# Kernel optimization log

Hardware: AMD Instinct MI355X
Metric: run time of the kernel (lower is better)

The kernel has to match this reference:

```python
import jax, jax.numpy as jnp
import numpy as np

NSLICES = 4
HID = 512
IN_DIM = 342   # input_shape - 1 (last column is phase)
OUT_DIM = 311
BATCH = 1024


def _cubic(y0, y1, y2, y3, mu):
    mu2 = mu * mu
    mu3 = mu2 * mu
    return ((-0.5 * y0 + 1.5 * y1 - 1.5 * y2 + 0.5 * y3) * mu3
            + (y0 - 2.5 * y1 + 2.0 * y2 - 0.5 * y3) * mu2
            + (-0.5 * y0 + 0.5 * y2) * mu
            + y1)


def setup_inputs() -> dict:
    key = jax.random.key(0)
    kx, k0, k1, k2 = jax.random.split(key, 4)
    x = jax.random.uniform(kx, (BATCH, IN_DIM + 1), dtype=jnp.float32)
    W0 = jax.random.normal(k0, (NSLICES, HID, IN_DIM), dtype=jnp.float32) * 0.1
    W1 = jax.random.normal(k1, (NSLICES, HID, HID), dtype=jnp.float32) * 0.1
    W2 = jax.random.normal(k2, (NSLICES, OUT_DIM, HID), dtype=jnp.float32) * 0.1
    b0 = jnp.zeros((NSLICES, HID), dtype=jnp.float32)
    b1 = jnp.zeros((NSLICES, HID), dtype=jnp.float32)
    b2 = jnp.zeros((NSLICES, OUT_DIM), dtype=jnp.float32)
    return {"x": x, "W0": W0, "W1": W1, "W2": W2, "b0": b0, "b1": b1, "b2": b2}


def reference(x, W0, W1, W2, b0, b1, b2):
    data, phase = x[:, :-1], x[:, -1]          # [B, 342], [B]
    pscale = NSLICES * phase                    # phase in [0,1) -> pscale in [0,4)
    mu = pscale % 1.0                           # [B]
    i1 = pscale.astype(jnp.int32) % NSLICES
    i0 = (i1 - 1) % NSLICES
    i2 = (i1 + 1) % NSLICES
    i3 = (i1 + 2) % NSLICES

    muW = mu[:, None, None]
    mub = mu[:, None]

    # Per-sample interpolated weights/biases (gather 4 slices + cubic blend)
    W0i = _cubic(W0[i0], W0[i1], W0[i2], W0[i3], muW)   # [B, 512, 342]
    W1i = _cubic(W1[i0], W1[i1], W1[i2], W1[i3], muW)   # [B, 512, 512]
    W2i = _cubic(W2[i0], W2[i1], W2[i2], W2[i3], muW)   # [B, 311, 512]
    b0i = _cubic(b0[i0], b0[i1], b0[i2], b0[i3], mub)   # [B, 512]
    b1i = _cubic(b1[i0], b1[i1], b1[i2], b1[i3], mub)   # [B, 512]
    b2i = _cubic(b2[i0], b2[i1], b2[i2], b2[i3], mub)   # [B, 311]

    # 3-layer MLP with per-sample weights (batched GEMV); dropout in eval mode (identity)
    H1 = jax.nn.elu(jnp.einsum('boi,bi->bo', W0i, data) + b0i)
    H2 = jax.nn.elu(jnp.einsum('boi,bi->bo', W1i, H1) + b1i)
    H3 = jnp.einsum('boi,bi->bo', W2i, H2) + b2i
    return H3
```

## Files before the change

### kernel.cpp

```cpp
#include <hip/hip_runtime.h>
#include <hip/hip_fp16.h>
#include <math.h>

typedef _Float16 f16x8 __attribute__((ext_vector_type(8)));
typedef float f32x4 __attribute__((ext_vector_type(4)));

#define NS 4
#define HID 512
#define IN_DIM 342
#define OUT_DIM 311
#define BATCH 1024
#define INP 352
#define K0V (NS*INP)
#define K12V (NS*HID)
#define XROW (IN_DIM+1)

#define OFF_ACOEF 0
#define OFF_X0H   4096
#define OFF_W0H   (OFF_X0H + 720896)
#define OFF_W1H   (OFF_W0H + 360448)
#define OFF_W2H   (OFF_W1H + 524288)
#define OFF_H1X   (OFF_W2H + 327680)
#define OFF_H2X   OFF_X0H

typedef __attribute__((address_space(3))) void lds_t;
typedef __attribute__((address_space(1))) const void gvm_t;
__device__ __forceinline__ void gload16(const void* g, void* l) {
    __builtin_amdgcn_global_load_lds((gvm_t*)g, (lds_t*)l, 16, 0, 0);
}

__global__ __launch_bounds__(256) void prep_all(
    const float* __restrict__ x,
    const float* __restrict__ W0, const float* __restrict__ W1,
    const float* __restrict__ W2,
    float* __restrict__ acoef,
    __half* __restrict__ X0h, __half* __restrict__ W0h,
    __half* __restrict__ W1h, __half* __restrict__ W2h)
{
    const int bid = blockIdx.x;
    const int t = threadIdx.x;
    if (bid < 512) {
        int o = bid;
        for (int k = t; k < K0V; k += 256) {
            int s = k / INP;
            int i = k - s*INP;
            float v = 0.f;
            if (i < IN_DIM) v = W0[((size_t)s*HID + o)*IN_DIM + i];
            W0h[(size_t)o*K0V + k] = __float2half(v);
        }
    } else if (bid < 1024) {
        int o = bid - 512;
        int k = t * 8;
        int s = k >> 9, i = k & 511;
        const float* src = W1 + ((size_t)s*HID + o)*HID + i;
        float4 v0 = *(const float4*)(src);
        float4 v1 = *(const float4*)(src + 4);
        f16x8 h;
        h[0]=(_Float16)v0.x; h[1]=(_Float16)v0.y; h[2]=(_Float16)v0.z; h[3]=(_Float16)v0.w;
        h[4]=(_Float16)v1.x; h[5]=(_Float16)v1.y; h[6]=(_Float16)v1.z; h[7]=(_Float16)v1.w;
        *(f16x8*)(W1h + (size_t)o*K12V + k) = h;
    } else if (bid < 1344) {
        int o = bid - 1024;
        int k = t * 8;
        int s = k >> 9, i = k & 511;
        f16x8 h = {};
        if (o < OUT_DIM) {
            const float* src = W2 + ((size_t)s*OUT_DIM + o)*HID + i;
            float4 v0 = *(const float4*)(src);
            float4 v1 = *(const float4*)(src + 4);
            h[0]=(_Float16)v0.x; h[1]=(_Float16)v0.y; h[2]=(_Float16)v0.z; h[3]=(_Float16)v0.w;
            h[4]=(_Float16)v1.x; h[5]=(_Float16)v1.y; h[6]=(_Float16)v1.z; h[7]=(_Float16)v1.w;
        }
        *(f16x8*)(W2h + (size_t)o*K12V + k) = h;
    } else {
        int b = bid - 1344;
        float phase = x[(size_t)b*XROW + IN_DIM];
        float ps = (float)NS * phase;
        float mu = ps - floorf(ps);
        int i1 = ((int)ps) & (NS-1);
        float mu2 = mu*mu, mu3 = mu2*mu;
        float c1 =  1.5f*mu3 - 2.5f*mu2 + 1.0f;
        float c2 = -1.5f*mu3 + 2.0f*mu2 + 0.5f*mu;
        float c3 =  0.5f*mu3 - 0.5f*mu2;
        float c0 = -0.5f*mu3 +      mu2 - 0.5f*mu;
        if (t < 4) {
            int rel = (t - i1) & 3;
            acoef[b*4 + t] = (rel==0)?c1:(rel==1)?c2:(rel==2)?c3:c0;
        }
        for (int k = t; k < K0V; k += 256) {
            int s = k / INP;
            int i = k - s*INP;
            int rel = (s - i1) & 3;
            float sel = (rel==0)?c1:(rel==1)?c2:(rel==2)?c3:c0;
            float v = (i < IN_DIM) ? x[(size_t)b*XROW + i] * sel : 0.f;
            X0h[(size_t)b*K0V + k] = __float2half(v);
        }
    }
}

template<int LAYER>
__global__ __launch_bounds__(256) void gemm_mfma(
    const __half* __restrict__ A,
    const __half* __restrict__ Bw,
    const float* __restrict__ acoef,
    const float* __restrict__ bias,
    __half* __restrict__ outH,
    float* __restrict__ outF)
{
    constexpr int K  = (LAYER==0) ? K0V : K12V;
    constexpr int NB = (LAYER==2) ? OUT_DIM : HID;
    constexpr int NITER = K / 64;

    __shared__ __align__(16) char lbuf[4][12288];

    const int t    = threadIdx.x;
    const int lane = t & 63;
    const int wid  = t >> 6;
    const int wm   = wid >> 1;
    const int wn   = wid & 1;
    const int m0   = blockIdx.y * 32;
    const int n0   = blockIdx.x * 64;

    const int rA = t >> 3, cA = t & 7;
    const __half* aSrc = A + (size_t)(m0 + rA)*K + ((cA ^ (rA & 7)) * 8);
    const __half* bSrc0 = Bw + (size_t)(n0 + rA)*K      + ((cA ^ (rA & 7)) * 8);
    const __half* bSrc1 = Bw + (size_t)(n0 + 32 + rA)*K + ((cA ^ (rA & 7)) * 8);
    const int wb = wid * 1024;

    f32x4 acc[2] = {};

    auto stage = [&](int it) {
        char* base = lbuf[it & 3];
        const int ko = it * 64;
        gload16(aSrc  + ko, base        + wb);
        gload16(bSrc0 + ko, base + 4096 + wb);
        gload16(bSrc1 + ko, base + 8192 + wb);
    };

    stage(0);
    stage(1);
    stage(2);

    for (int it = 0; it < NITER; ++it) {
        if (it + 2 < NITER)      asm volatile("s_waitcnt vmcnt(6)" ::: "memory");
        else if (it + 1 < NITER) asm volatile("s_waitcnt vmcnt(3)" ::: "memory");
        else                     asm volatile("s_waitcnt vmcnt(0)" ::: "memory");
        __builtin_amdgcn_s_barrier();
        __builtin_amdgcn_sched_barrier(0);
        if (it + 3 < NITER) stage(it + 3);
        const char* sA = lbuf[it & 3];
        const char* sB = sA + 4096;
        #pragma unroll
        for (int kk = 0; kk < 2; ++kk) {
            const int kb = kk*64 + (lane>>4)*16;
            const int rr = wm*16 + (lane&15);
            f16x8 af = *(const f16x8*)(sA + rr*128 + (kb ^ ((rr&7)<<4)));
            #pragma unroll
            for (int ni = 0; ni < 2; ++ni) {
                const int oo = wn*32 + ni*16 + (lane&15);
                f16x8 bf = *(const f16x8*)(sB + oo*128 + (kb ^ ((oo&7)<<4)));
                acc[ni] = __builtin_amdgcn_mfma_f32_16x16x32_f16(af, bf, acc[ni], 0, 0, 0);
            }
        }
    }

    #pragma unroll
    for (int r = 0; r < 4; ++r) {
        const int row = m0 + wm*16 + (lane>>4)*4 + r;
        const float c0 = acoef[row*4+0], c1 = acoef[row*4+1],
                    c2 = acoef[row*4+2], c3 = acoef[row*4+3];
        #pragma unroll
        for (int ni = 0; ni < 2; ++ni) {
            const int col = n0 + wn*32 + ni*16 + (lane&15);
            float v = acc[ni][r];
            if (LAYER == 2) {
                if (col < OUT_DIM) {
                    float bi = c0*bias[col] + c1*bias[NB+col]
                             + c2*bias[2*NB+col] + c3*bias[3*NB+col];
                    outF[(size_t)row*OUT_DIM + col] = v + bi;
                }
            } else {
                float bi = c0*bias[col] + c1*bias[NB+col]
                         + c2*bias[2*NB+col] + c3*bias[3*NB+col];
                v += bi;
                v = (v > 0.f) ? v : expm1f(v);
                size_t o = (size_t)row*K12V + col;
                outH[o        ] = __float2half(c0*v);
                outH[o +   HID] = __float2half(c1*v);
                outH[o + 2*HID] = __float2half(c2*v);
                outH[o + 3*HID] = __float2half(c3*v);
            }
        }
    }
}

extern "C" void kernel_launch(void* const* d_in, const int* in_sizes, int n_in,
                              void* d_out, int out_size, void* d_ws, size_t ws_size,
                              hipStream_t stream) {
    const float* x  = (const float*)d_in[0];
    const float* W0 = (const float*)d_in[1];
    const float* W1 = (const float*)d_in[2];
    const float* W2 = (const float*)d_in[3];
    const float* b0 = (const float*)d_in[4];
    const float* b1 = (const float*)d_in[5];
    const float* b2 = (const float*)d_in[6];
    float* out = (float*)d_out;
    float* ws  = (float*)d_ws;

    float*  acoef = ws + OFF_ACOEF;
    __half* X0h   = (__half*)(ws + OFF_X0H);
    __half* W0h   = (__half*)(ws + OFF_W0H);
    __half* W1h   = (__half*)(ws + OFF_W1H);
    __half* W2h   = (__half*)(ws + OFF_W2H);
    __half* H1x   = (__half*)(ws + OFF_H1X);
    __half* H2x   = (__half*)(ws + OFF_H2X);

    prep_all<<<dim3(2368), dim3(256), 0, stream>>>(x, W0, W1, W2, acoef,
                                                   X0h, W0h, W1h, W2h);

    gemm_mfma<0><<<dim3(HID/64, BATCH/32), dim3(256), 0, stream>>>(
        X0h, W0h, acoef, b0, H1x, nullptr);
    gemm_mfma<1><<<dim3(HID/64, BATCH/32), dim3(256), 0, stream>>>(
        H1x, W1h, acoef, b1, H2x, nullptr);
    gemm_mfma<2><<<dim3(320/64, BATCH/32), dim3(256), 0, stream>>>(
        H2x, W2h, acoef, b2, nullptr, out);
}
```

Baseline: 41.87 us.

## Use 8 waves per GEMM block, each computing one 16x16 MFMA tile

The GEMM blocks grow from 4 to 8 wavefronts with the same 32x64 output tile, so each wave now owns one 16x16 accumulator instead of two. Loading is split by role: waves 0-3 stage the A tile and waves 4-7 stage the B tile, and the per-wave vmcnt waits are changed to match. The aim is more waves per CU for latency hiding on this small, latency-bound problem. In exchange there are more barriers per unit of work, less ILP per wave, and uneven load issue between the two wave groups.

Result: slower. 43.27 us (+3.3%).

```diff
diff --git a/kernel.cpp b/kernel.cpp
--- a/kernel.cpp
+++ b/kernel.cpp
@@ -99,7 +99,7 @@
 }
 
 template<int LAYER>
-__global__ __launch_bounds__(256) void gemm_mfma(
+__global__ __launch_bounds__(512) void gemm_mfma(
     const __half* __restrict__ A,
     const __half* __restrict__ Bw,
     const float* __restrict__ acoef,
@@ -116,25 +116,29 @@
     const int t    = threadIdx.x;
     const int lane = t & 63;
     const int wid  = t >> 6;
-    const int wm   = wid >> 1;
-    const int wn   = wid & 1;
+    const int wm   = wid >> 2;
+    const int wn   = wid & 3;
     const int m0   = blockIdx.y * 32;
     const int n0   = blockIdx.x * 64;
 
-    const int rA = t >> 3, cA = t & 7;
-    const __half* aSrc = A + (size_t)(m0 + rA)*K + ((cA ^ (rA & 7)) * 8);
-    const __half* bSrc0 = Bw + (size_t)(n0 + rA)*K      + ((cA ^ (rA & 7)) * 8);
-    const __half* bSrc1 = Bw + (size_t)(n0 + 32 + rA)*K + ((cA ^ (rA & 7)) * 8);
-    const int wb = wid * 1024;
-
-    f32x4 acc[2] = {};
+    const int rl = lane >> 3;
+    const int cl = lane & 7;
+    const int widb = (wid >= 4) ? wid - 4 : 0;
+    const __half* aSrc  = A  + (size_t)(m0 + wid*8 + rl)*K        + ((cl ^ rl) * 8);
+    const __half* bSrc0 = Bw + (size_t)(n0 + widb*16 + rl)*K      + ((cl ^ rl) * 8);
+    const __half* bSrc1 = Bw + (size_t)(n0 + widb*16 + 8 + rl)*K  + ((cl ^ rl) * 8);
+
+    f32x4 acc = {};
 
     auto stage = [&](int it) {
         char* base = lbuf[it & 3];
         const int ko = it * 64;
-        gload16(aSrc  + ko, base        + wb);
-        gload16(bSrc0 + ko, base + 4096 + wb);
-        gload16(bSrc1 + ko, base + 8192 + wb);
+        if (wid < 4) {
+            gload16(aSrc + ko, base + wid*1024);
+        } else {
+            gload16(bSrc0 + ko, base + 4096 + widb*2048);
+            gload16(bSrc1 + ko, base + 4096 + widb*2048 + 1024);
+        }
     };
 
     stage(0);
@@ -142,9 +146,15 @@
     stage(2);
 
     for (int it = 0; it < NITER; ++it) {
-        if (it + 2 < NITER)      asm volatile("s_waitcnt vmcnt(6)" ::: "memory");
-        else if (it + 1 < NITER) asm volatile("s_waitcnt vmcnt(3)" ::: "memory");
-        else                     asm volatile("s_waitcnt vmcnt(0)" ::: "memory");
+        if (it + 2 < NITER) {
+            if (wid < 4) asm volatile("s_waitcnt vmcnt(2)" ::: "memory");
+            else         asm volatile("s_waitcnt vmcnt(4)" ::: "memory");
+        } else if (it + 1 < NITER) {
+            if (wid < 4) asm volatile("s_waitcnt vmcnt(1)" ::: "memory");
+            else         asm volatile("s_waitcnt vmcnt(2)" ::: "memory");
+        } else {
+            asm volatile("s_waitcnt vmcnt(0)" ::: "memory");
+        }
         __builtin_amdgcn_s_barrier();
         __builtin_amdgcn_sched_barrier(0);
         if (it + 3 < NITER) stage(it + 3);
@@ -155,12 +165,9 @@
             const int kb = kk*64 + (lane>>4)*16;
             const int rr = wm*16 + (lane&15);
             f16x8 af = *(const f16x8*)(sA + rr*128 + (kb ^ ((rr&7)<<4)));
-            #pragma unroll
-            for (int ni = 0; ni < 2; ++ni) {
-                const int oo = wn*32 + ni*16 + (lane&15);
-                f16x8 bf = *(const f16x8*)(sB + oo*128 + (kb ^ ((oo&7)<<4)));
-                acc[ni] = __builtin_amdgcn_mfma_f32_16x16x32_f16(af, bf, acc[ni], 0, 0, 0);
-            }
+            const int oo = wn*16 + (lane&15);
+            f16x8 bf = *(const f16x8*)(sB + oo*128 + (kb ^ ((oo&7)<<4)));
+            acc = __builtin_amdgcn_mfma_f32_16x16x32_f16(af, bf, acc, 0, 0, 0);
         }
     }
 
@@ -169,27 +176,24 @@
         const int row = m0 + wm*16 + (lane>>4)*4 + r;
         const float c0 = acoef[row*4+0], c1 = acoef[row*4+1],
                     c2 = acoef[row*4+2], c3 = acoef[row*4+3];
-        #pragma unroll
-        for (int ni = 0; ni < 2; ++ni) {
-            const int col = n0 + wn*32 + ni*16 + (lane&15);
-            float v = acc[ni][r];
-            if (LAYER == 2) {
-                if (col < OUT_DIM) {
-                    float bi = c0*bias[col] + c1*bias[NB+col]
-                             + c2*bias[2*NB+col] + c3*bias[3*NB+col];
-                    outF[(size_t)row*OUT_DIM + col] = v + bi;
-                }
-            } else {
+        const int col = n0 + wn*16 + (lane&15);
+        float v = acc[r];
+        if (LAYER == 2) {
+            if (col < OUT_DIM) {
                 float bi = c0*bias[col] + c1*bias[NB+col]
                          + c2*bias[2*NB+col] + c3*bias[3*NB+col];
-                v += bi;
-                v = (v > 0.f) ? v : expm1f(v);
-                size_t o = (size_t)row*K12V + col;
-                outH[o        ] = __float2half(c0*v);
-                outH[o +   HID] = __float2half(c1*v);
-                outH[o + 2*HID] = __float2half(c2*v);
-                outH[o + 3*HID] = __float2half(c3*v);
+                outF[(size_t)row*OUT_DIM + col] = v + bi;
             }
+        } else {
+            float bi = c0*bias[col] + c1*bias[NB+col]
+                     + c2*bias[2*NB+col] + c3*bias[3*NB+col];
+            v += bi;
+            v = (v > 0.f) ? v : expm1f(v);
+            size_t o = (size_t)row*K12V + col;
+            outH[o        ] = __float2half(c0*v);
+            outH[o +   HID] = __float2half(c1*v);
+            outH[o + 2*HID] = __float2half(c2*v);
+            outH[o + 3*HID] = __float2half(c3*v);
         }
     }
 }
@@ -218,10 +222,10 @@
     prep_all<<<dim3(2368), dim3(256), 0, stream>>>(x, W0, W1, W2, acoef,
                                                    X0h, W0h, W1h, W2h);
 
-    gemm_mfma<0><<<dim3(HID/64, BATCH/32), dim3(256), 0, stream>>>(
+    gemm_mfma<0><<<dim3(HID/64, BATCH/32), dim3(512), 0, stream>>>(
         X0h, W0h, acoef, b0, H1x, nullptr);
-    gemm_mfma<1><<<dim3(HID/64, BATCH/32), dim3(256), 0, stream>>>(
+    gemm_mfma<1><<<dim3(HID/64, BATCH/32), dim3(512), 0, stream>>>(
         H1x, W1h, acoef, b1, H2x, nullptr);
-    gemm_mfma<2><<<dim3(320/64, BATCH/32), dim3(256), 0, stream>>>(
+    gemm_mfma<2><<<dim3(320/64, BATCH/32), dim3(512), 0, stream>>>(
         H2x, W2h, acoef, b2, nullptr, out);
 }
```
